# Kernel optimization log

Measured on AMD Instinct MI355X. Metric: run time of the kernel, lower is better.

Reference implementation:

```python
import jax, jax.numpy as jnp
import numpy as np

N = 6144          # active voxels / points
C = 96            # embed_channels
B = 2             # batch size
D = H = W = 32    # sparse spatial shape
K = 16            # PFAS kNN
DEPTH = 4
GRID_OPTS = np.array([[0.1, 0.1, 0.1], [0.4, 0.4, 0.4], [0.2, 0.2, 0.2]], dtype=np.float32)
BN_EPS = 1e-5


def _bn(x, g, b):
    # BatchNorm1d in training mode: batch stats over the point dim, biased var
    m = x.mean(0)
    v = jnp.var(x, axis=0)
    return (x - m) * jax.lax.rsqrt(v + BN_EPS) * g + b


def _seg_sum(x, seg):
    return jax.ops.segment_sum(x, seg, num_segments=N)


def _forward(indices, x, fp_w, fp_b, fp_g, fp_be, att_w1, att_b1, att_w2, att_b2,
             ff_w1, ff_b1, ff_g, ff_be, ff_w2, ff_b2, sa_w1, sa_b1, sa_w2, sa_b2,
             fj_w1, fj_b1, fj_g, fj_be, fj_w2, fj_b2,
             proj_w, proj_g, proj_be, lw_w, lw_g, lw_be, w_w, adp_w,
             fuse_w, fuse_g, fuse_be, conv1_w, bn1_g, bn1_be, conv2_w, bn2_g, bn2_be):
    # ---- CMPFE ----
    p = jax.nn.relu(_bn(x @ fp_w.T + fp_b, fp_g, fp_be))            # [N,9]
    cd, cl, nm = p[:, :3], p[:, 3:6], p[:, 6:9]

    def _att(f, i):
        h = jax.nn.relu(f @ att_w1[i].T + att_b1[i])
        return jax.nn.sigmoid(h @ att_w2[i].T + att_b2[i])

    enh = jnp.concatenate([cd, cl * _att(cl, 0), nm * _att(nm, 1)], axis=1)
    fu = jax.nn.relu(_bn(enh @ ff_w1.T + ff_b1, ff_g, ff_be)) @ ff_w2.T + ff_b2
    sem = jax.nn.sigmoid(jax.nn.relu(fu @ sa_w1.T + sa_b1) @ sa_w2.T + sa_b2)
    feat = fu * sem + x * (1.0 - sem)                               # new x.features

    # ---- PFAS: kNN geometry stats ----
    coord = indices[:, 1:].astype(jnp.float32)                      # [N,3]
    batch = indices[:, 0]
    sq = jnp.sum(coord * coord, axis=1)
    d2 = sq[:, None] + sq[None, :] - 2.0 * (coord @ coord.T)
    dist = jnp.sqrt(jnp.maximum(d2, 1e-12))
    same = batch[None, :] == batch[:, None]
    eye = jnp.eye(N, dtype=bool)
    dist = jnp.where(same & ~eye, dist, jnp.inf)
    neg_nd, idx = jax.lax.top_k(-dist, K)                           # K nearest
    nbr = coord[idx]                                                # [N,K,3]
    cent = nbr - nbr.mean(axis=1, keepdims=True)
    cov = jnp.einsum('nkd,nke->nde', cent, cent) / (K - 1)
    S = jnp.linalg.svd(cov, compute_uv=False)                       # [N,3] descending
    Sn = S / (S.sum(axis=1, keepdims=True) + 1e-6)
    linearity = Sn[:, 0:1] - (Sn[:, 1] + Sn[:, 2])[:, None]
    mean_dist = (-neg_nd).mean(axis=1, keepdims=True)
    density = 1.0 / (mean_dist + 1e-6)
    fl = jax.nn.relu(_bn(feat @ fj_w1.T + fj_b1, fj_g, fj_be)) @ fj_w2.T + fj_b2
    fp_ = jax.nn.softmax(fl, axis=1)
    tower = (density * 2.0 + fp_[:, 0:1]) / 3.0
    backg = (jnp.maximum(1.0 - linearity, 1.0 - density) + fp_[:, 1:2]) / 3.0
    line = (linearity * 2.0 + fp_[:, 2:3]) / 3.0
    go = jnp.asarray(GRID_OPTS)
    lg = go[2] * jnp.array([1.0, 1.0, 5.0], jnp.float32)            # last dim *5
    grid_sizes = tower * go[0] + backg * go[1] + line * lg + 1e-6   # [N,3]

    # ---- representative grids (N > 200 path) ----
    gm = grid_sizes.mean(axis=1)
    order = jnp.argsort(gm)
    reps = [grid_sizes[order[100:200]].mean(0),
            grid_sizes[order[::-1][:100]].mean(0),
            grid_sizes[order[:100]].mean(0)]

    # ---- voxel-grid clustering (torch_geometric voxel_grid + unique inverse) ----
    start = coord.min(axis=0)

    def _cluster(size):
        size = jnp.clip(size, 1e-6, None)
        c = jnp.clip(jnp.floor((coord - start) / size).astype(jnp.int64), 0, 4095)
        mx = c.max(axis=0) + 1
        ids = ((batch.astype(jnp.int64) * mx[0] + c[:, 0]) * mx[1] + c[:, 1]) * mx[2] + c[:, 2]
        _, inv = jnp.unique(ids, return_inverse=True, size=N, fill_value=0)
        return inv.reshape(-1)

    # ---- adaptive multi-branch scatter softmax aggregation ----
    branch_feats = []
    for i in range(DEPTH - 1):
        seg = _cluster(reps[i])
        cnt = jnp.maximum(_seg_sum(jnp.ones((N, 1), feat.dtype), seg), 1.0)
        pw = jax.nn.relu(_bn(feat @ lw_w[i].T, lw_g[i], lw_be[i]))
        pw = pw - (_seg_sum(pw, seg) / cnt)[seg]
        pw = pw @ w_w[i].T
        pw = jnp.exp(pw - pw.max())
        pw = pw / (_seg_sum(pw, seg)[seg] + 1e-6)
        pf = jax.nn.relu(_bn(feat @ proj_w[i].T, proj_g[i], proj_be[i])) * pw
        branch_feats.append(_seg_sum(pf, seg)[seg])
    adp = jax.nn.softmax(feat @ adp_w.T, axis=1)                    # [N,3]
    agg = jnp.einsum('nc,ncd->nd', adp, jnp.stack(branch_feats, 1))
    last = jax.nn.relu(_bn(feat @ proj_w[-1].T, proj_g[-1], proj_be[-1]))
    fused = jax.nn.relu(_bn(jnp.concatenate([last, agg], 1) @ fuse_w.T, fuse_g, fuse_be)) + feat
    res = fused

    # ---- submanifold sparse conv block (dense scatter form; inactive sites zero,
    #      outputs gathered only at active sites == SubMConv3d) ----
    bi, zi, yi, xi = indices[:, 0], indices[:, 1], indices[:, 2], indices[:, 3]

    def _subm(f, w):
        grid = jnp.zeros((B, D, H, W, C), f.dtype).at[bi, zi, yi, xi].set(f)
        o = jax.lax.conv_general_dilated(grid, w, (1, 1, 1), 'SAME',
                                         dimension_numbers=('NDHWC', 'DHWIO', 'NDHWC'))
        return o[bi, zi, yi, xi]

    f1 = jax.nn.relu(_bn(_subm(fused, conv1_w), bn1_g, bn1_be))
    f2 = _bn(_subm(f1, conv2_w), bn2_g, bn2_be)
    return jax.nn.relu(f2 + res)


def setup_inputs() -> dict:
    key = jax.random.key(0)
    ks = iter(jax.random.split(key, 64))

    def rn(*shape, s=0.05):
        return jax.random.normal(next(ks), shape, jnp.float32) * s

    # unique active voxel coordinates
    rng = np.random.default_rng(0)
    flat = rng.choice(B * D * H * W, size=N, replace=False)
    b = flat // (D * H * W)
    r = flat % (D * H * W)
    z = r // (H * W)
    y = (r % (H * W)) // W
    xw = r % W
    indices = jnp.asarray(np.stack([b, z, y, xw], 1).astype(np.int32))
    Ch = C // 2
    return {
        'x': jax.random.normal(next(ks), (N, C), jnp.float32),
        'indices': indices,
        'fp_w': rn(9, C), 'fp_b': rn(9), 'fp_g': jnp.ones(9), 'fp_be': jnp.zeros(9),
        'att_w1': rn(2, 16, 3), 'att_b1': rn(2, 16), 'att_w2': rn(2, 3, 16), 'att_b2': rn(2, 3),
        'ff_w1': rn(C, 9), 'ff_b1': rn(C), 'ff_g': jnp.ones(C), 'ff_be': jnp.zeros(C),
        'ff_w2': rn(C, C), 'ff_b2': rn(C),
        'sa_w1': rn(Ch, C), 'sa_b1': rn(Ch), 'sa_w2': rn(1, Ch), 'sa_b2': rn(1),
        'fj_w1': rn(64, C), 'fj_b1': rn(64), 'fj_g': jnp.ones(64), 'fj_be': jnp.zeros(64),
        'fj_w2': rn(3, 64), 'fj_b2': rn(3),
        'proj_w': rn(DEPTH, C, C), 'proj_g': jnp.ones((DEPTH, C)), 'proj_be': jnp.zeros((DEPTH, C)),
        'lw_w': rn(DEPTH - 1, C, C), 'lw_g': jnp.ones((DEPTH - 1, C)), 'lw_be': jnp.zeros((DEPTH - 1, C)),
        'w_w': rn(DEPTH - 1, C, C),
        'adp_w': rn(DEPTH - 1, C),
        'fuse_w': rn(C, 2 * C), 'fuse_g': jnp.ones(C), 'fuse_be': jnp.zeros(C),
        'conv1_w': rn(3, 3, 3, C, C), 'bn1_g': jnp.ones(C), 'bn1_be': jnp.zeros(C),
        'conv2_w': rn(3, 3, 3, C, C), 'bn2_g': jnp.ones(C), 'bn2_be': jnp.zeros(C),
    }


def reference(x, indices, fp_w, fp_b, fp_g, fp_be, att_w1, att_b1, att_w2, att_b2,
              ff_w1, ff_b1, ff_g, ff_be, ff_w2, ff_b2, sa_w1, sa_b1, sa_w2, sa_b2,
              fj_w1, fj_b1, fj_g, fj_be, fj_w2, fj_b2,
              proj_w, proj_g, proj_be, lw_w, lw_g, lw_be, w_w, adp_w,
              fuse_w, fuse_g, fuse_be, conv1_w, bn1_g, bn1_be, conv2_w, bn2_g, bn2_be):
    return _forward(indices, x, fp_w, fp_b, fp_g, fp_be, att_w1, att_b1, att_w2, att_b2,
                    ff_w1, ff_b1, ff_g, ff_be, ff_w2, ff_b2, sa_w1, sa_b1, sa_w2, sa_b2,
                    fj_w1, fj_b1, fj_g, fj_be, fj_w2, fj_b2,
                    proj_w, proj_g, proj_be, lw_w, lw_g, lw_be, w_w, adp_w,
                    fuse_w, fuse_g, fuse_be, conv1_w, bn1_g, bn1_be, conv2_w, bn2_g, bn2_be)
```

## Files before the change

### kernel.cpp

```cpp
#include <hip/hip_runtime.h>
#include <cstdint>

#define NPTS 6144
#define CH 96
#define NCELEM (NPTS*CH)
#define HTSZ 16384

__device__ __forceinline__ unsigned fenc(float f){
  unsigned u = __float_as_uint(f);
  return (u & 0x80000000u) ? ~u : (u | 0x80000000u);
}
__device__ __forceinline__ float fdec(unsigned u){
  unsigned b = (u & 0x80000000u) ? (u & 0x7FFFFFFFu) : ~u;
  return __uint_as_float(b);
}

__device__ void eig3(double a00,double a01,double a02,double a11,double a12,double a22,
                     double &e0,double &e1,double &e2){
  double p1 = a01*a01 + a02*a02 + a12*a12;
  double q = (a00+a11+a22)/3.0;
  double b00=a00-q, b11=a11-q, b22=a22-q;
  double p2 = b00*b00 + b11*b11 + b22*b22 + 2.0*p1;
  if (p2 <= 1e-300){ e0=e1=e2=q; return; }
  double pp = sqrt(p2/6.0);
// ... 300 lines not shown
            for (int t=15;t>0;--t){
              unsigned a = s[t-1], b = s[t];
              unsigned lo = a<b?a:b, hi = a<b?b:a;
              s[t-1]=lo; s[t]=hi;
            }
          }
        }
      }
    }
  }
  for (int m=32; m; m>>=1) cnt += __shfl_xor(cnt, m);
  if (cnt < 16){
    #pragma unroll
    for (int t=0;t<16;++t) s[t] = 0xFFFFFFFFu;
    for (int it=0; it<96; ++it){
      int j = lane + it*64;
      unsigned pc = pk[j];
      if (j != pid && (int)(pc>>15) == myb){
        int dz = (int)((pc>>10)&31) - mz;
        int dy = (int)((pc>>5)&31) - my_;
        int dx = (int)(pc&31) - mx_;
        unsigned d2 = (unsigned)(dz*dz + dy*dy + dx*dx);
        unsigned key = (d2<<13) | (unsigned)j;
        if (key < s[15]){
          s[15] = key;
          #pragma unroll
          for (int t=15;t>0;--t){
            unsigned a = s[t-1], b = s[t];
            unsigned lo = a<b?a:b, hi = a<b?b:a;
            s[t-1]=lo; s[t]=hi;
          }
        }
      }
    }
  }
  float sdist = 0.f;
  int sz=0,sy=0,sx=0,szz=0,syy=0,sxx=0,szy=0,szx=0,syx=0;
  for (int r=0;r<16;++r){
    unsigned m = s[0];
    #pragma unroll
    for (int w=32; w; w>>=1){
      unsigned o = (unsigned)__shfl_xor((int)m, w);
      m = m<o ? m : o;
    }
    bool own = (s[0] == m);
    #pragma unroll
    for (int t=0;t<15;++t) s[t] = own ? s[t+1] : s[t];
    if (own) s[15] = 0xFFFFFFFFu;
    unsigned idx = m & 8191u;
    unsigned d2 = m >> 13;
    sdist += sqrtf((float)d2);
    unsigned pc = pk[idx];
    int nz=(int)((pc>>10)&31), ny=(int)((pc>>5)&31), nx=(int)(pc&31);
    sz+=nz; sy+=ny; sx+=nx;
    szz+=nz*nz; syy+=ny*ny; sxx+=nx*nx; szy+=nz*ny; szx+=nz*nx; syx+=ny*nx;
  }
  if (lane == 0){
    double m0 = sz/16.0, m1 = sy/16.0, m2 = sx/16.0;
    float c00 = (float)(((double)szz - 16.0*m0*m0)/15.0);
    float c11 = (float)(((double)syy - 16.0*m1*m1)/15.0);
    float c22 = (float)(((double)sxx - 16.0*m2*m2)/15.0);
    float c01 = (float)(((double)szy - 16.0*m0*m1)/15.0);
    float c02 = (float)(((double)szx - 16.0*m0*m2)/15.0);
    float c12 = (float)(((double)syx - 16.0*m1*m2)/15.0);
    double e0,e1,e2;
    eig3((double)c00,(double)c01,(double)c02,(double)c11,(double)c12,(double)c22, e0,e1,e2);
    float s0 = (float)fabs(e0), s1 = (float)fabs(e1), s2 = (float)fabs(e2);
    float den = s0 + s1 + s2 + 1e-6f;
    float sn0 = s0/den, sn1 = s1/den, sn2 = s2/den;
    linearity[pid] = sn0 - (sn1 + sn2);
    float md = sdist * (1.f/16.f);
    density[pid] = 1.f/(md + 1e-6f);
  }
}

__global__ void k_geo(const float* __restrict__ t64, const float* __restrict__ st,
                      const float* __restrict__ fg, const float* __restrict__ fbe,
                      const float* __restrict__ w2, const float* __restrict__ b2,
                      const float* __restrict__ density, const float* __restrict__ linearity,
                      float* __restrict__ gsz, float* __restrict__ gm){
  int p = blockIdx.x*blockDim.x + threadIdx.x;
  if (p >= NPTS) return;
  float fl[3];
  #pragma unroll
  for (int o=0;o<3;++o) fl[o] = b2[o];
  for (int k=0;k<64;++k){
    float v = t64[(long)p*64+k];
    v = fmaxf((v - st[k*2])*st[k*2+1]*fg[k] + fbe[k], 0.f);
    #pragma unroll
    for (int o=0;o<3;++o) fl[o] = fmaf(v, w2[o*64+k], fl[o]);
  }
  float mx = fmaxf(fl[0], fmaxf(fl[1], fl[2]));
  float e0 = expf(fl[0]-mx), e1 = expf(fl[1]-mx), e2 = expf(fl[2]-mx);
  float es = e0+e1+e2;
  float p0 = e0/es, p1 = e1/es, p2 = e2/es;
  float den = density[p], lin = linearity[p];
  float tw = (den*2.f + p0)/3.f;
  float bg = (fmaxf(1.f-lin, 1.f-den) + p1)/3.f;
  float ln = (lin*2.f + p2)/3.f;
  float g0 = tw*0.1f + bg*0.4f + ln*0.2f + 1e-6f;
  float g1 = tw*0.1f + bg*0.4f + ln*0.2f + 1e-6f;
  float g2 = tw*0.1f + bg*0.4f + ln*1.0f + 1e-6f;
  gsz[p*3+0]=g0; gsz[p*3+1]=g1; gsz[p*3+2]=g2;
  gm[p] = (g0+g1+g2)/3.f;
}

#define RNKCHUNK 768
__global__ void __launch_bounds__(256) k_rank(const float* __restrict__ gm, int* __restrict__ rank){
  __shared__ unsigned long long lk[RNKCHUNK];
  int j0 = blockIdx.y*RNKCHUNK;
  for (int i=threadIdx.x; i<RNKCHUNK; i+=256){
    int j = j0 + i;
    lk[i] = (((unsigned long long)fenc(gm[j]))<<13) | (unsigned long long)j;
  }
  __syncthreads();
  int p = blockIdx.x*256 + threadIdx.x;
  unsigned long long myk = (((unsigned long long)fenc(gm[p]))<<13) | (unsigned long long)p;
  int cnt = 0;
  #pragma unroll 4
  for (int i=0; i<RNKCHUNK; ++i) cnt += (lk[i] < myk) ? 1 : 0;
  atomicAdd(&rank[p], cnt);
}
__global__ void k_scatter(const int* __restrict__ rank, const float* __restrict__ gsz,
                          float* __restrict__ bkt){
  int p = blockIdx.x*blockDim.x + threadIdx.x;
  if (p >= NPTS) return;
  int r = rank[p];
  int z = -1, t = 0;
  if (r < 100){ z = 2; t = r; }
  else if (r < 200){ z = 0; t = r - 100; }
  else if (r >= NPTS-100){ z = 1; t = r - (NPTS-100); }
  if (z >= 0){
    #pragma unroll
    for (int d=0; d<3; ++d) bkt[(z*100 + t)*3 + d] = gsz[p*3+d];
  }
}
__global__ void k_reps(const float* __restrict__ bkt, float* __restrict__ reps){
  int i = threadIdx.x;
  if (i >= 9) return;
  int z = i/3, d = i - z*3;
  double s = 0.0;
  for (int t=0; t<100; ++t) s += (double)bkt[(z*100 + t)*3 + d];
  reps[i] = (float)(s/100.0);
}

__global__ void k_cluster_c(const int* __restrict__ ind, const float* __restrict__ reps,
                            const int* __restrict__ startmin, int* __restrict__ cbuf, int* mxbuf){
  int z = blockIdx.y;
  int p = blockIdx.x*blockDim.x + threadIdx.x;
  __shared__ int lmx[3];
  if (threadIdx.x < 3) lmx[threadIdx.x] = 0;
  __syncthreads();
  if (p < NPTS){
    #pragma unroll
    for (int d=0; d<3; ++d){
      float sizev = fmaxf(reps[z*3+d], 1e-6f);
      float cf = floorf(((float)ind[p*4+1+d] - (float)startmin[d]) / sizev);
      int ci = (int)cf;
      ci = ci < 0 ? 0 : (ci > 4095 ? 4095 : ci);
      cbuf[((long)z*NPTS + p)*3 + d] = ci;
      atomicMax(&lmx[d], ci);
    }
  }
  __syncthreads();
  if (threadIdx.x < 3) atomicMax(&mxbuf[z*3+threadIdx.x], lmx[threadIdx.x]);
}
__global__ void k_cluster_ids(const int* __restrict__ ind, const int* __restrict__ cbuf,
                              const int* __restrict__ mxbuf, long long* __restrict__ ids){
  int z = blockIdx.y;
  int p = blockIdx.x*blockDim.x + threadIdx.x;
  if (p >= NPTS) return;
  long long mx0 = mxbuf[z*3+0]+1, mx1 = mxbuf[z*3+1]+1, mx2 = mxbuf[z*3+2]+1;
  long long b = ind[p*4];
  const int* cc = cbuf + ((long)z*NPTS + p)*3;
  ids[(long)z*NPTS + p] = ((b*mx0 + cc[0])*mx1 + cc[1])*mx2 + cc[2];
}

__device__ __forceinline__ int ht_hash(unsigned long long id){
  unsigned long long h = id * 0x9E3779B97F4A7C15ull;
  return (int)(h >> 49) & (HTSZ-1);
}
__global__ void k_seg_build(const long long* __restrict__ ids,
                            unsigned long long* __restrict__ keys, int* __restrict__ vals){
  int z = blockIdx.y;
  int p = blockIdx.x*blockDim.x + threadIdx.x;
  if (p >= NPTS) return;
  unsigned long long id = (unsigned long long)ids[(long)z*NPTS + p];
  unsigned long long* K = keys + (long)z*HTSZ;
  int* V = vals + (long)z*HTSZ;
  int slot = ht_hash(id);
  while (true){
    unsigned long long prev = atomicCAS(&K[slot], ~0ull, id);
    if (prev == ~0ull || prev == id){ atomicMin(&V[slot], p); break; }
    slot = (slot + 1) & (HTSZ-1);
  }
}
__global__ void k_seg_lookup(const long long* __restrict__ ids,
                             const unsigned long long* __restrict__ keys, const int* __restrict__ vals,
                             int* __restrict__ seg, int* __restrict__ cnt){
  int z = blockIdx.y;
  int p = blockIdx.x*blockDim.x + threadIdx.x;
  if (p >= NPTS) return;
  unsigned long long id = (unsigned long long)ids[(long)z*NPTS + p];
  const unsigned long long* K = keys + (long)z*HTSZ;
  int slot = ht_hash(id);
  while (K[slot] != id) slot = (slot + 1) & (HTSZ-1);
  int rep = vals[(long)z*HTSZ + slot];
  seg[(long)z*NPTS + p] = rep;
  atomicAdd(&cnt[(long)z*NPTS + rep], 1);
}

__global__ void k_pw_accum(const float* __restrict__ tlw, const float* __restrict__ stats,
                           const float* __restrict__ g, const float* __restrict__ be,
                           const int* __restrict__ seg, float* __restrict__ S){
  int z = blockIdx.y;
  int idx = blockIdx.x*blockDim.x + threadIdx.x;
  int p = idx/CH, c = idx - p*CH;
  const float* st = stats + z*192;
  float v = tlw[(long)z*NCELEM + idx];
  v = fmaxf((v - st[c*2])*st[c*2+1]*g[z*CH+c] + be[z*CH+c], 0.f);
  atomicAdd(&S[(long)z*NCELEM + (long)seg[(long)z*NPTS+p]*CH + c], v);
}
__global__ void k_exp_accum(const float* __restrict__ pw2, const unsigned* __restrict__ maxenc,
                            const int* __restrict__ seg, float* __restrict__ E){
  int z = blockIdx.y;
  int idx = blockIdx.x*blockDim.x + threadIdx.x;
  int p = idx/CH, c = idx - p*CH;
  float mv = fdec(maxenc[z]);
  float v = expf(pw2[(long)z*NCELEM + idx] - mv);
  atomicAdd(&E[(long)z*NCELEM + (long)seg[(long)z*NPTS+p]*CH + c], v);
}
__global__ void k_pf_accum(const float* __restrict__ tp, const float* __restrict__ stats,
                           const float* __restrict__ pg, const float* __restrict__ pbe,
                           const float* __restrict__ pw2, const unsigned* __restrict__ maxenc,
                           const int* __restrict__ seg, const float* __restrict__ E,
                           float* __restrict__ F){
  int z = blockIdx.y;
  int idx = blockIdx.x*blockDim.x + threadIdx.x;
  int p = idx/CH, c = idx - p*CH;
  const float* st = stats + z*192;
  float v = tp[(long)z*NCELEM + idx];
  v = fmaxf((v - st[c*2])*st[c*2+1]*pg[z*CH+c] + pbe[z*CH+c], 0.f);
  float mv = fdec(maxenc[z]);
  int sg = seg[(long)z*NPTS+p];
  float w = expf(pw2[(long)z*NCELEM + idx] - mv) / (E[(long)z*NCELEM + (long)sg*CH + c] + 1e-6f);
  atomicAdd(&F[(long)z*NCELEM + (long)sg*CH + c], v*w);
}
__global__ void k_adp(const float* __restrict__ feat, const float* __restrict__ aw,
                      float* __restrict__ adp){
  int p = blockIdx.x*blockDim.x + threadIdx.x;
  if (p >= NPTS) return;
  float a0=0.f, a1=0.f, a2=0.f;
  for (int k=0;k<CH;++k){
    float f = feat[(long)p*CH+k];
    a0 = fmaf(f, aw[k], a0);
    a1 = fmaf(f, aw[CH+k], a1);
    a2 = fmaf(f, aw[2*CH+k], a2);
  }
  float m = fmaxf(a0, fmaxf(a1,a2));
  float e0 = expf(a0-m), e1 = expf(a1-m), e2 = expf(a2-m);
  float s = e0+e1+e2;
  adp[p*3]=e0/s; adp[p*3+1]=e1/s; adp[p*3+2]=e2/s;
}
__global__ void k_agg(const float* __restrict__ adp, const float* __restrict__ F,
                      const int* __restrict__ seg, float* __restrict__ agg){
  int idx = blockIdx.x*blockDim.x + threadIdx.x;
  int p = idx/CH, c = idx - p*CH;
  float s = 0.f;
  #pragma unroll
  for (int z=0;z<3;++z)
    s = fmaf(adp[p*3+z], F[(long)z*NCELEM + (long)seg[(long)z*NPTS+p]*CH + c], s);
  agg[idx] = s;
}

__global__ void k_fused(const float* __restrict__ tf, const float* __restrict__ st,
                        const float* __restrict__ fg, const float* __restrict__ fbe,
                        const float* __restrict__ feat, float* __restrict__ fused){
  int idx = blockIdx.x*blockDim.x + threadIdx.x;
  int c = idx % CH;
  float v = tf[idx];
  v = fmaxf((v - st[c*2])*st[c*2+1]*fg[c] + fbe[c], 0.f);
  fused[idx] = v + feat[idx];
}
__global__ void k_table(const int* __restrict__ ind, int* __restrict__ table){
  int p = blockIdx.x*blockDim.x + threadIdx.x;
  if (p >= NPTS) return;
  int b = ind[p*4], z = ind[p*4+1], y = ind[p*4+2], x = ind[p*4+3];
  table[((b*32+z)*32+y)*32+x] = p;
}
__global__ void k_nbr(const int* __restrict__ ind, const int* __restrict__ table,
                      int* __restrict__ nbrtab){
  int idx = blockIdx.x*blockDim.x + threadIdx.x;
  if (idx >= NPTS*27) return;
  int p = idx/27, tap = idx - p*27;
  int dz = tap/9 - 1;
  int rm = tap % 9;
  int dy = rm/3 - 1, dx = rm%3 - 1;
  int b = ind[p*4], z = ind[p*4+1]+dz, y = ind[p*4+2]+dy, x = ind[p*4+3]+dx;
  int q = -1;
  if ((unsigned)z < 32u && (unsigned)y < 32u && (unsigned)x < 32u)
    q = table[((b*32+z)*32+y)*32+x];
  nbrtab[idx] = q;
}
__global__ void __launch_bounds__(256) k_convlist(const int* __restrict__ nbrtab,
                                                  int* __restrict__ tapcnt,
                                                  int* __restrict__ ptlist){
  __shared__ int lcnt[27], lbase[27], lpos[27];
  int tid = threadIdx.x;
  if (tid < 27){ lcnt[tid] = 0; lpos[tid] = 0; }
  __syncthreads();
  int base = blockIdx.x * 6912;
  for (int i = tid; i < 6912; i += 256){
    int idx = base + i;
    if (nbrtab[idx] >= 0) atomicAdd(&lcnt[idx % 27], 1);
  }
  __syncthreads();
  if (tid < 27) lbase[tid] = atomicAdd(&tapcnt[tid], lcnt[tid]);
  __syncthreads();
  for (int i = tid; i < 6912; i += 256){
    int idx = base + i;
    int q = nbrtab[idx];
    if (q >= 0){
      int tap = idx % 27;
      int p = idx / 27;
      int pos = lbase[tap] + atomicAdd(&lpos[tap], 1);
      ptlist[tap*NPTS + pos] = (p<<16) | q;
    }
  }
}
__global__ void __launch_bounds__(256) k_conv_gemm(
    const float* __restrict__ src, const float* __restrict__ Wc,
    const int* __restrict__ tapcnt, const int* __restrict__ ptlist,
    float* __restrict__ out){
  int tap = blockIdx.y;
  int n = tapcnt[tap];
  int r0 = blockIdx.x*32;
  if (r0 >= n) return;
  __shared__ float Al[32*97];
  __shared__ float Wl[96*97];
  __shared__ int pqs[32];
  int tid = threadIdx.x;
  if (tid < 32){
    int r = r0 + tid;
    pqs[tid] = (r < n) ? ptlist[tap*NPTS + r] : -1;
  }
  __syncthreads();
  for (int idx4 = tid; idx4 < 2304; idx4 += 256){
    int ci = idx4/24, c4 = idx4 - ci*24;
    float4 w = ((const float4*)(Wc + ((long)tap*96 + ci)*96))[c4];
    float* d = &Wl[ci*97 + c4*4];
    d[0]=w.x; d[1]=w.y; d[2]=w.z; d[3]=w.w;
  }
  for (int idx4 = tid; idx4 < 32*24; idx4 += 256){
    int ir = idx4/24, c4 = idx4 - ir*24;
    int pq = pqs[ir];
    float4 s = make_float4(0.f,0.f,0.f,0.f);
    if (pq >= 0){
      int q = pq & 0xFFFF;
      s = ((const float4*)(src + (long)q*CH))[c4];
    }
    float* d = &Al[ir*97 + c4*4];
    d[0]=s.x; d[1]=s.y; d[2]=s.z; d[3]=s.w;
  }
  __syncthreads();
  int rp = tid >> 4, cg = tid & 15;
  int co0 = cg*6;
  int ra = 2*rp, rb = ra+1;
  float acc0[6]={0,0,0,0,0,0}, acc1[6]={0,0,0,0,0,0};
  for (int k=0;k<96;++k){
    float a0 = Al[ra*97+k], a1 = Al[rb*97+k];
    #pragma unroll
    for (int j=0;j<6;++j){
      float w = Wl[k*97+co0+j];
      acc0[j] = fmaf(a0, w, acc0[j]);
      acc1[j] = fmaf(a1, w, acc1[j]);
    }
  }
  int pa = pqs[ra], pb = pqs[rb];
  if (pa >= 0){
    float* o = out + (long)(pa>>16)*CH + co0;
    #pragma unroll
    for (int j=0;j<6;++j) atomicAdd(&o[j], acc0[j]);
  }
  if (pb >= 0){
    float* o = out + (long)(pb>>16)*CH + co0;
    #pragma unroll
    for (int j=0;j<6;++j) atomicAdd(&o[j], acc1[j]);
  }
}
__global__ void k_bnrelu(const float* __restrict__ a, const float* __restrict__ st,
                         const float* __restrict__ g, const float* __restrict__ be,
                         float* __restrict__ o){
  int idx = blockIdx.x*blockDim.x + threadIdx.x;
  int c = idx % CH;
  float v = a[idx];
  o[idx] = fmaxf((v - st[c*2])*st[c*2+1]*g[c] + be[c], 0.f);
}
__global__ void k_final(const float* __restrict__ c2, const float* __restrict__ st,
                        const float* __restrict__ g, const float* __restrict__ be,
                        const float* __restrict__ fused, float* __restrict__ out){
  int idx = blockIdx.x*blockDim.x + threadIdx.x;
  int c = idx % CH;
  float v = c2[idx];
  v = (v - st[c*2])*st[c*2+1]*g[c] + be[c];
  out[idx] = fmaxf(v + fused[idx], 0.f);
}

extern "C" void kernel_launch(void* const* d_in, const int* in_sizes, int n_in,
                              void* d_out, int out_size, void* d_ws, size_t ws_size,
                              hipStream_t stream)
{
  const float* x      = (const float*)d_in[0];
  const int*   ind    = (const int*)  d_in[1];
  const float* fp_w   = (const float*)d_in[2];
  const float* fp_b   = (const float*)d_in[3];
  const float* fp_g   = (const float*)d_in[4];
  const float* fp_be  = (const float*)d_in[5];
  const float* att_w1 = (const float*)d_in[6];
  const float* att_b1 = (const float*)d_in[7];
  const float* att_w2 = (const float*)d_in[8];
  const float* att_b2 = (const float*)d_in[9];
  const float* ff_w1  = (const float*)d_in[10];
  const float* ff_b1  = (const float*)d_in[11];
  const float* ff_g   = (const float*)d_in[12];
  const float* ff_be  = (const float*)d_in[13];
  const float* ff_w2  = (const float*)d_in[14];
  const float* ff_b2  = (const float*)d_in[15];
  const float* sa_w1  = (const float*)d_in[16];
  const float* sa_b1  = (const float*)d_in[17];
  const float* sa_w2  = (const float*)d_in[18];
  const float* sa_b2  = (const float*)d_in[19];
  const float* fj_w1  = (const float*)d_in[20];
  const float* fj_b1  = (const float*)d_in[21];
  const float* fj_g   = (const float*)d_in[22];
  const float* fj_be  = (const float*)d_in[23];
  const float* fj_w2  = (const float*)d_in[24];
  const float* fj_b2  = (const float*)d_in[25];
  const float* proj_w = (const float*)d_in[26];
  const float* proj_g = (const float*)d_in[27];
  const float* proj_be= (const float*)d_in[28];
  const float* lw_w   = (const float*)d_in[29];
  const float* lw_g   = (const float*)d_in[30];
  const float* lw_be  = (const float*)d_in[31];
  const float* w_w    = (const float*)d_in[32];
  const float* adp_w  = (const float*)d_in[33];
  const float* fuse_w = (const float*)d_in[34];
  const float* fuse_g = (const float*)d_in[35];
  const float* fuse_be= (const float*)d_in[36];
  const float* conv1_w= (const float*)d_in[37];
  const float* bn1_g  = (const float*)d_in[38];
  const float* bn1_be = (const float*)d_in[39];
  const float* conv2_w= (const float*)d_in[40];
  const float* bn2_g  = (const float*)d_in[41];
  const float* bn2_be = (const float*)d_in[42];
  float* outp = (float*)d_out;
  (void)in_sizes; (void)n_in; (void)out_size; (void)ws_size;

  char* ws = (char*)d_ws;
  size_t off = 0;
  auto alloc = [&](size_t bytes)->size_t{
    off = (off + 255) & ~(size_t)255;
    size_t o = off; off += bytes; return o;
  };
  const size_t FNC = (size_t)NCELEM*4;
  size_t o_packed = alloc((size_t)NPTS*4);
  size_t o_start  = alloc(16);
  size_t o_dens   = alloc((size_t)NPTS*4);
  size_t o_lin    = alloc((size_t)NPTS*4);
  size_t o_t9     = alloc((size_t)NPTS*9*4);
  size_t o_enh    = alloc((size_t)NPTS*9*4);
  size_t o_gm     = alloc((size_t)NPTS*4);
  size_t o_gsz    = alloc((size_t)NPTS*3*4);
  size_t o_reps   = alloc(16*4);
  size_t o_bkt    = alloc((size_t)3*100*3*4);
  size_t o_cbuf   = alloc((size_t)3*NPTS*3*4);
  size_t o_ids    = alloc((size_t)3*NPTS*8);
  size_t o_seg    = alloc((size_t)3*NPTS*4);
  size_t o_adp    = alloc((size_t)NPTS*3*4);
  size_t o_table  = alloc((size_t)65536*4);
  size_t o_nbr    = alloc((size_t)NPTS*27*4);
  size_t o_ptlist = alloc((size_t)27*NPTS*4);
  size_t o_t64    = alloc((size_t)NPTS*64*4);
  size_t o_stats  = alloc((size_t)13*192*4);
  size_t o_htk    = alloc((size_t)3*HTSZ*8);
  size_t o_htv    = alloc((size_t)3*HTSZ*4);
  size_t o_S      = alloc(3*FNC);
  size_t o_E      = alloc(3*FNC);
  size_t o_F      = alloc(3*FNC);
  size_t o_c1     = alloc(FNC);
  size_t o_c2     = alloc(FNC);
  size_t o_cnt    = alloc((size_t)3*NPTS*4);
  size_t o_rank   = alloc((size_t)NPTS*4);
  size_t o_tapcnt = alloc(32*4);
  size_t o_mx     = alloc(16*4);
  size_t o_maxenc = alloc(16*4);
  size_t zend = off;
  size_t o_T96 = alloc(FNC);
  size_t o_fu  = alloc(FNC);
  size_t o_feat= alloc(FNC);
  size_t o_tlw = alloc(3*FNC);
  size_t o_pw2 = alloc(3*FNC);
  size_t o_tp  = alloc(4*FNC);
  size_t o_agg = alloc(FNC);
  size_t o_tf  = alloc(FNC);
  size_t o_fsd = alloc(FNC);
  size_t o_f1  = alloc(FNC);

  float* stats = (float*)(ws + o_stats);
  long zcount = (long)((zend - o_S)/4);

  k_zero<<<dim3(2048), dim3(256), 0, stream>>>((int*)(ws+o_S), zcount);
  k_init<<<dim3(256), dim3(256), 0, stream>>>((int*)(ws+o_table), (int*)(ws+o_start));
  k_htinit<<<dim3((3*HTSZ+255)/256), dim3(256), 0, stream>>>((unsigned long long*)(ws+o_htk), (int*)(ws+o_htv));
  k_pack_min<<<dim3(24), dim3(256), 0, stream>>>(ind, (unsigned*)(ws+o_packed), (int*)(ws+o_start));
  k_table<<<dim3(24), 256, 0, stream>>>(ind, (int*)(ws+o_table));

  k_mm<<<dim3(192,1), 256, 0, stream>>>(x, fp_w, fp_b, (float*)(ws+o_t9), 96, 9,
      0,0,0,0, nullptr,0, nullptr,nullptr,0, nullptr,nullptr,nullptr, nullptr, 0);
  k_stats<<<dim3(9,1), 256, 0, stream>>>((float*)(ws+o_t9), 0, 9, stats+0*192, 0);
  k_p_att_enh<<<dim3(24), 256, 0, stream>>>((float*)(ws+o_t9), stats+0*192, fp_g, fp_be,
      att_w1, att_b1, att_w2, att_b2, (float*)(ws+o_enh));

  k_mm<<<dim3(192,1), 256, 0, stream>>>((float*)(ws+o_enh), ff_w1, ff_b1, (float*)(ws+o_T96), 9, 96,
      0,0,0,0, nullptr,0, nullptr,nullptr,0, nullptr,nullptr,nullptr, nullptr, 0);
  k_stats<<<dim3(96,1), 256, 0, stream>>>((float*)(ws+o_T96), 0, 96, stats+1*192, 0);
  k_mm<<<dim3(192,1), 256, 0, stream>>>((float*)(ws+o_T96), ff_w2, ff_b2, (float*)(ws+o_fu), 96, 96,
      0,0,0,0, stats+1*192,0, ff_g, ff_be,0, nullptr,nullptr,nullptr, nullptr, 1);

  k_sem_feat<<<dim3(1536), 256, 0, stream>>>((float*)(ws+o_fu), x, sa_w1, sa_b1, sa_w2, sa_b2,
      (float*)(ws+o_feat));

  k_knn<<<dim3(1536), 256, 0, stream>>>((unsigned*)(ws+o_packed), (int*)(ws+o_table),
      (float*)(ws+o_dens), (float*)(ws+o_lin));

  k_mm<<<dim3(192,1), 256, 0, stream>>>((float*)(ws+o_feat), fj_w1, fj_b1, (float*)(ws+o_t64), 96, 64,
      0,0,0,0, nullptr,0, nullptr,nullptr,0, nullptr,nullptr,nullptr, nullptr, 0);
  k_stats<<<dim3(64,1), 256, 0, stream>>>((float*)(ws+o_t64), 0, 64, stats+2*192, 0);
  k_geo<<<dim3(24), 256, 0, stream>>>((float*)(ws+o_t64), stats+2*192, fj_g, fj_be, fj_w2, fj_b2,
      (float*)(ws+o_dens), (float*)(ws+o_lin), (float*)(ws+o_gsz), (float*)(ws+o_gm));

  k_rank<<<dim3(24,8), 256, 0, stream>>>((float*)(ws+o_gm), (int*)(ws+o_rank));
  k_scatter<<<dim3(24), 256, 0, stream>>>((int*)(ws+o_rank), (float*)(ws+o_gsz), (float*)(ws+o_bkt));
  k_reps<<<dim3(1), 64, 0, stream>>>((float*)(ws+o_bkt), (float*)(ws+o_reps));

  k_cluster_c<<<dim3(24,3), 256, 0, stream>>>(ind, (float*)(ws+o_reps), (int*)(ws+o_start),
      (int*)(ws+o_cbuf), (int*)(ws+o_mx));
  k_cluster_ids<<<dim3(24,3), 256, 0, stream>>>(ind, (int*)(ws+o_cbuf), (int*)(ws+o_mx),
      (long long*)(ws+o_ids));
  k_seg_build<<<dim3(24,3), 256, 0, stream>>>((long long*)(ws+o_ids),
      (unsigned long long*)(ws+o_htk), (int*)(ws+o_htv));
  k_seg_lookup<<<dim3(24,3), 256, 0, stream>>>((long long*)(ws+o_ids),
      (unsigned long long*)(ws+o_htk), (int*)(ws+o_htv), (int*)(ws+o_seg), (int*)(ws+o_cnt));

  k_mm<<<dim3(192,3), 256, 0, stream>>>((float*)(ws+o_feat), lw_w, nullptr, (float*)(ws+o_tlw), 96, 96,
      0, 96*96, NCELEM, 0, nullptr,0, nullptr,nullptr,0, nullptr,nullptr,nullptr, nullptr, 0);
  k_stats<<<dim3(96,3), 256, 0, stream>>>((float*)(ws+o_tlw), NCELEM, 96, stats+3*192, 192);
  k_pw_accum<<<dim3(2304,3), 256, 0, stream>>>((float*)(ws+o_tlw), stats+3*192, lw_g, lw_be,
      (int*)(ws+o_seg), (float*)(ws+o_S));
  k_mm<<<dim3(192,3), 256, 0, stream>>>((float*)(ws+o_tlw), w_w, nullptr, (float*)(ws+o_pw2), 96, 96,
      NCELEM, 96*96, NCELEM, 0, stats+3*192,192, lw_g, lw_be,96,
      (float*)(ws+o_S), (int*)(ws+o_seg), (int*)(ws+o_cnt), (unsigned*)(ws+o_maxenc), 2);
  k_exp_accum<<<dim3(2304,3), 256, 0, stream>>>((float*)(ws+o_pw2), (unsigned*)(ws+o_maxenc),
      (int*)(ws+o_seg), (float*)(ws+o_E));
  k_mm<<<dim3(192,4), 256, 0, stream>>>((float*)(ws+o_feat), proj_w, nullptr, (float*)(ws+o_tp), 96, 96,
      0, 96*96, NCELEM, 0, nullptr,0, nullptr,nullptr,0, nullptr,nullptr,nullptr, nullptr, 0);
  k_stats<<<dim3(96,4), 256, 0, stream>>>((float*)(ws+o_tp), NCELEM, 96, stats+6*192, 192);
  k_pf_accum<<<dim3(2304,3), 256, 0, stream>>>((float*)(ws+o_tp), stats+6*192, proj_g, proj_be,
      (float*)(ws+o_pw2), (unsigned*)(ws+o_maxenc), (int*)(ws+o_seg), (float*)(ws+o_E), (float*)(ws+o_F));
  k_adp<<<dim3(24), 256, 0, stream>>>((float*)(ws+o_feat), adp_w, (float*)(ws+o_adp));
  k_agg<<<dim3(2304), 256, 0, stream>>>((float*)(ws+o_adp), (float*)(ws+o_F), (int*)(ws+o_seg),
      (float*)(ws+o_agg));

  k_mm_fuse<<<dim3(192), 256, 0, stream>>>((float*)(ws+o_tp) + (size_t)3*NCELEM, stats+9*192,
      proj_g + 3*96, proj_be + 3*96, (float*)(ws+o_agg), fuse_w, (float*)(ws+o_tf));
  k_stats<<<dim3(96,1), 256, 0, stream>>>((float*)(ws+o_tf), 0, 96, stats+10*192, 0);
  k_fused<<<dim3(2304), 256, 0, stream>>>((float*)(ws+o_tf), stats+10*192, fuse_g, fuse_be,
      (float*)(ws+o_feat), (float*)(ws+o_fsd));

  k_nbr<<<dim3((NPTS*27+255)/256), 256, 0, stream>>>(ind, (int*)(ws+o_table), (int*)(ws+o_nbr));
  k_convlist<<<dim3(24), 256, 0, stream>>>((int*)(ws+o_nbr), (int*)(ws+o_tapcnt),
      (int*)(ws+o_ptlist));
  k_conv_gemm<<<dim3(192,27), 256, 0, stream>>>((float*)(ws+o_fsd), conv1_w,
      (int*)(ws+o_tapcnt), (int*)(ws+o_ptlist), (float*)(ws+o_c1));
  k_stats<<<dim3(96,1), 256, 0, stream>>>((float*)(ws+o_c1), 0, 96, stats+11*192, 0);
  k_bnrelu<<<dim3(2304), 256, 0, stream>>>((float*)(ws+o_c1), stats+11*192, bn1_g, bn1_be, (float*)(ws+o_f1));
  k_conv_gemm<<<dim3(192,27), 256, 0, stream>>>((float*)(ws+o_f1), conv2_w,
      (int*)(ws+o_tapcnt), (int*)(ws+o_ptlist), (float*)(ws+o_c2));
  k_stats<<<dim3(96,1), 256, 0, stream>>>((float*)(ws+o_c2), 0, 96, stats+12*192, 0);
  k_final<<<dim3(2304), 256, 0, stream>>>((float*)(ws+o_c2), stats+12*192, bn2_g, bn2_be,
      (float*)(ws+o_fsd), outp);
}
```

Measured before the change: 543.9 us.

## Replace scatter-atomic tap-list sparse conv with output-stationary gather conv

The sparse 3x3x3 convolution no longer builds per-tap point lists and scatters results with float atomics. Each block now owns 16 output points, loops over all 27 taps, gathers neighbour rows and the tap weight slice into shared memory, and accumulates in registers before a plain store. This removes the list-building kernel, the atomics and the zeroing of the conv outputs, which now sit outside the zeroed region. The cost is that every block reloads the full 96x96 weight slice for each active tap, giving far more weight traffic, and the grid shrinks to 384 blocks with one row per thread.

```diff
diff --git a/kernel.cpp b/kernel.cpp
--- a/kernel.cpp
+++ b/kernel.cpp
@@ -626,91 +626,54 @@
     q = table[((b*32+z)*32+y)*32+x];
   nbrtab[idx] = q;
 }
-__global__ void __launch_bounds__(256) k_convlist(const int* __restrict__ nbrtab,
-                                                  int* __restrict__ tapcnt,
-                                                  int* __restrict__ ptlist){
-  __shared__ int lcnt[27], lbase[27], lpos[27];
+__global__ void __launch_bounds__(256) k_conv_os(
+    const float* __restrict__ src, const float* __restrict__ Wc,
+    const int* __restrict__ nbrtab, float* __restrict__ out){
+  __shared__ float Al[16*97];
+  __shared__ float Wl[96*97];
+  __shared__ int qrow[16];
+  __shared__ int anyv;
   int tid = threadIdx.x;
-  if (tid < 27){ lcnt[tid] = 0; lpos[tid] = 0; }
-  __syncthreads();
-  int base = blockIdx.x * 6912;
-  for (int i = tid; i < 6912; i += 256){
-    int idx = base + i;
-    if (nbrtab[idx] >= 0) atomicAdd(&lcnt[idx % 27], 1);
-  }
-  __syncthreads();
-  if (tid < 27) lbase[tid] = atomicAdd(&tapcnt[tid], lcnt[tid]);
-  __syncthreads();
-  for (int i = tid; i < 6912; i += 256){
-    int idx = base + i;
-    int q = nbrtab[idx];
-    if (q >= 0){
-      int tap = idx % 27;
-      int p = idx / 27;
-      int pos = lbase[tap] + atomicAdd(&lpos[tap], 1);
-      ptlist[tap*NPTS + pos] = (p<<16) | q;
-    }
-  }
-}
-__global__ void __launch_bounds__(256) k_conv_gemm(
-    const float* __restrict__ src, const float* __restrict__ Wc,
-    const int* __restrict__ tapcnt, const int* __restrict__ ptlist,
-    float* __restrict__ out){
-  int tap = blockIdx.y;
-  int n = tapcnt[tap];
-  int r0 = blockIdx.x*32;
-  if (r0 >= n) return;
-  __shared__ float Al[32*97];
-  __shared__ float Wl[96*97];
-  __shared__ int pqs[32];
-  int tid = threadIdx.x;
-  if (tid < 32){
-    int r = r0 + tid;
-    pqs[tid] = (r < n) ? ptlist[tap*NPTS + r] : -1;
-  }
-  __syncthreads();
-  for (int idx4 = tid; idx4 < 2304; idx4 += 256){
-    int ci = idx4/24, c4 = idx4 - ci*24;
-    float4 w = ((const float4*)(Wc + ((long)tap*96 + ci)*96))[c4];
-    float* d = &Wl[ci*97 + c4*4];
-    d[0]=w.x; d[1]=w.y; d[2]=w.z; d[3]=w.w;
-  }
-  for (int idx4 = tid; idx4 < 32*24; idx4 += 256){
-    int ir = idx4/24, c4 = idx4 - ir*24;
-    int pq = pqs[ir];
-    float4 s = make_float4(0.f,0.f,0.f,0.f);
-    if (pq >= 0){
-      int q = pq & 0xFFFF;
-      s = ((const float4*)(src + (long)q*CH))[c4];
-    }
-    float* d = &Al[ir*97 + c4*4];
-    d[0]=s.x; d[1]=s.y; d[2]=s.z; d[3]=s.w;
-  }
-  __syncthreads();
+  int p0 = blockIdx.x*16;
   int rp = tid >> 4, cg = tid & 15;
   int co0 = cg*6;
-  int ra = 2*rp, rb = ra+1;
-  float acc0[6]={0,0,0,0,0,0}, acc1[6]={0,0,0,0,0,0};
-  for (int k=0;k<96;++k){
-    float a0 = Al[ra*97+k], a1 = Al[rb*97+k];
-    #pragma unroll
-    for (int j=0;j<6;++j){
-      float w = Wl[k*97+co0+j];
-      acc0[j] = fmaf(a0, w, acc0[j]);
-      acc1[j] = fmaf(a1, w, acc1[j]);
-    }
-  }
-  int pa = pqs[ra], pb = pqs[rb];
-  if (pa >= 0){
-    float* o = out + (long)(pa>>16)*CH + co0;
-    #pragma unroll
-    for (int j=0;j<6;++j) atomicAdd(&o[j], acc0[j]);
-  }
-  if (pb >= 0){
-    float* o = out + (long)(pb>>16)*CH + co0;
-    #pragma unroll
-    for (int j=0;j<6;++j) atomicAdd(&o[j], acc1[j]);
-  }
+  float acc[6] = {0,0,0,0,0,0};
+  for (int tap=0; tap<27; ++tap){
+    if (tid == 0) anyv = 0;
+    __syncthreads();
+    if (tid < 16){
+      int q = nbrtab[(p0+tid)*27 + tap];
+      qrow[tid] = q;
+      if (q >= 0) atomicOr(&anyv, 1);
+    }
+    __syncthreads();
+    if (anyv){
+      for (int i4 = tid; i4 < 2304; i4 += 256){
+        int ci = i4/24, c4 = i4 - ci*24;
+        float4 w = ((const float4*)(Wc + ((long)tap*96 + ci)*96))[c4];
+        float* d = &Wl[ci*97 + c4*4];
+        d[0]=w.x; d[1]=w.y; d[2]=w.z; d[3]=w.w;
+      }
+      for (int i4 = tid; i4 < 16*24; i4 += 256){
+        int ir = i4/24, c4 = i4 - ir*24;
+        int q = qrow[ir];
+        float4 s = make_float4(0.f,0.f,0.f,0.f);
+        if (q >= 0) s = ((const float4*)(src + (long)q*CH))[c4];
+        float* d = &Al[ir*97 + c4*4];
+        d[0]=s.x; d[1]=s.y; d[2]=s.z; d[3]=s.w;
+      }
+      __syncthreads();
+      for (int k=0;k<96;++k){
+        float a = Al[rp*97+k];
+        #pragma unroll
+        for (int j=0;j<6;++j) acc[j] = fmaf(a, Wl[k*97+co0+j], acc[j]);
+      }
+      __syncthreads();
+    }
+  }
+  float* o = out + (long)(p0+rp)*CH + co0;
+  #pragma unroll
+  for (int j=0;j<6;++j) o[j] = acc[j];
 }
 __global__ void k_bnrelu(const float* __restrict__ a, const float* __restrict__ st,
                          const float* __restrict__ g, const float* __restrict__ be,
@@ -803,7 +766,6 @@
   size_t o_adp    = alloc((size_t)NPTS*3*4);
   size_t o_table  = alloc((size_t)65536*4);
   size_t o_nbr    = alloc((size_t)NPTS*27*4);
-  size_t o_ptlist = alloc((size_t)27*NPTS*4);
   size_t o_t64    = alloc((size_t)NPTS*64*4);
   size_t o_stats  = alloc((size_t)13*192*4);
   size_t o_htk    = alloc((size_t)3*HTSZ*8);
@@ -811,11 +773,8 @@
   size_t o_S      = alloc(3*FNC);
   size_t o_E      = alloc(3*FNC);
   size_t o_F      = alloc(3*FNC);
-  size_t o_c1     = alloc(FNC);
-  size_t o_c2     = alloc(FNC);
   size_t o_cnt    = alloc((size_t)3*NPTS*4);
   size_t o_rank   = alloc((size_t)NPTS*4);
-  size_t o_tapcnt = alloc(32*4);
   size_t o_mx     = alloc(16*4);
   size_t o_maxenc = alloc(16*4);
   size_t zend = off;
@@ -828,7 +787,9 @@
   size_t o_agg = alloc(FNC);
   size_t o_tf  = alloc(FNC);
   size_t o_fsd = alloc(FNC);
+  size_t o_c1  = alloc(FNC);
   size_t o_f1  = alloc(FNC);
+  size_t o_c2  = alloc(FNC);
 
   float* stats = (float*)(ws + o_stats);
   long zcount = (long)((zend - o_S)/4);
@@ -902,14 +863,12 @@
       (float*)(ws+o_feat), (float*)(ws+o_fsd));
 
   k_nbr<<<dim3((NPTS*27+255)/256), 256, 0, stream>>>(ind, (int*)(ws+o_table), (int*)(ws+o_nbr));
-  k_convlist<<<dim3(24), 256, 0, stream>>>((int*)(ws+o_nbr), (int*)(ws+o_tapcnt),
-      (int*)(ws+o_ptlist));
-  k_conv_gemm<<<dim3(192,27), 256, 0, stream>>>((float*)(ws+o_fsd), conv1_w,
-      (int*)(ws+o_tapcnt), (int*)(ws+o_ptlist), (float*)(ws+o_c1));
+  k_conv_os<<<dim3(NPTS/16), 256, 0, stream>>>((float*)(ws+o_fsd), conv1_w,
+      (int*)(ws+o_nbr), (float*)(ws+o_c1));
   k_stats<<<dim3(96,1), 256, 0, stream>>>((float*)(ws+o_c1), 0, 96, stats+11*192, 0);
   k_bnrelu<<<dim3(2304), 256, 0, stream>>>((float*)(ws+o_c1), stats+11*192, bn1_g, bn1_be, (float*)(ws+o_f1));
-  k_conv_gemm<<<dim3(192,27), 256, 0, stream>>>((float*)(ws+o_f1), conv2_w,
-      (int*)(ws+o_tapcnt), (int*)(ws+o_ptlist), (float*)(ws+o_c2));
+  k_conv_os<<<dim3(NPTS/16), 256, 0, stream>>>((float*)(ws+o_f1), conv2_w,
+      (int*)(ws+o_nbr), (float*)(ws+o_c2));
   k_stats<<<dim3(96,1), 256, 0, stream>>>((float*)(ws+o_c2), 0, 96, stats+12*192, 0);
   k_final<<<dim3(2304), 256, 0, stream>>>((float*)(ws+o_c2), stats+12*192, bn2_g, bn2_be,
       (float*)(ws+o_fsd), outp);
```

New measurement: 767.8 us. 41.2% more time.

## Replace atomic scatter in sparse conv with per-tap partial buffer and gather-sum

Applied to the files above, without the earlier changes.

The sparse 3x3x3 convolution GEMM now writes each tap's output row into a dedicated [point, tap, channel] partial buffer instead of atomically adding into the output. A new gather kernel then sums the valid taps per point using the neighbour table. This removes float atomics and the zeroing pass, and makes the sum order deterministic. In exchange it writes and rereads a 27x-sized intermediate (about 64 MB), with an atomic fallback when the workspace is too small.

```diff
diff --git a/kernel.cpp b/kernel.cpp
--- a/kernel.cpp
+++ b/kernel.cpp
@@ -653,6 +653,81 @@
   }
 }
 __global__ void __launch_bounds__(256) k_conv_gemm(
+    const float* __restrict__ src, const float* __restrict__ Wc,
+    const int* __restrict__ tapcnt, const int* __restrict__ ptlist,
+    float* __restrict__ part){
+  int tap = blockIdx.y;
+  int n = tapcnt[tap];
+  int r0 = blockIdx.x*32;
+  if (r0 >= n) return;
+  __shared__ float Al[32*97];
+  __shared__ float Wl[96*97];
+  __shared__ int pqs[32];
+  int tid = threadIdx.x;
+  if (tid < 32){
+    int r = r0 + tid;
+    pqs[tid] = (r < n) ? ptlist[tap*NPTS + r] : -1;
+  }
+  __syncthreads();
+  for (int idx4 = tid; idx4 < 2304; idx4 += 256){
+    int ci = idx4/24, c4 = idx4 - ci*24;
+    float4 w = ((const float4*)(Wc + ((long)tap*96 + ci)*96))[c4];
+    float* d = &Wl[ci*97 + c4*4];
+    d[0]=w.x; d[1]=w.y; d[2]=w.z; d[3]=w.w;
+  }
+  for (int idx4 = tid; idx4 < 32*24; idx4 += 256){
+    int ir = idx4/24, c4 = idx4 - ir*24;
+    int pq = pqs[ir];
+    float4 s = make_float4(0.f,0.f,0.f,0.f);
+    if (pq >= 0){
+      int q = pq & 0xFFFF;
+      s = ((const float4*)(src + (long)q*CH))[c4];
+    }
+    float* d = &Al[ir*97 + c4*4];
+    d[0]=s.x; d[1]=s.y; d[2]=s.z; d[3]=s.w;
+  }
+  __syncthreads();
+  int rp = tid >> 4, cg = tid & 15;
+  int co0 = cg*6;
+  int ra = 2*rp, rb = ra+1;
+  float acc0[6]={0,0,0,0,0,0}, acc1[6]={0,0,0,0,0,0};
+  for (int k=0;k<96;++k){
+    float a0 = Al[ra*97+k], a1 = Al[rb*97+k];
+    #pragma unroll
+    for (int j=0;j<6;++j){
+      float w = Wl[k*97+co0+j];
+      acc0[j] = fmaf(a0, w, acc0[j]);
+      acc1[j] = fmaf(a1, w, acc1[j]);
+    }
+  }
+  int pa = pqs[ra], pb = pqs[rb];
+  if (pa >= 0){
+    float* o = part + ((long)(pa>>16)*27 + tap)*CH + co0;
+    #pragma unroll
+    for (int j=0;j<6;++j) o[j] = acc0[j];
+  }
+  if (pb >= 0){
+    float* o = part + ((long)(pb>>16)*27 + tap)*CH + co0;
+    #pragma unroll
+    for (int j=0;j<6;++j) o[j] = acc1[j];
+  }
+}
+__global__ void __launch_bounds__(256) k_conv_sum(const int* __restrict__ nbrtab,
+                                                  const float* __restrict__ part,
+                                                  float* __restrict__ out){
+  int idx = blockIdx.x*256 + threadIdx.x;
+  int p = idx/24, c4 = idx - p*24;
+  const int* nt = nbrtab + p*27;
+  float4 acc = make_float4(0.f,0.f,0.f,0.f);
+  for (int tap=0; tap<27; ++tap){
+    if (nt[tap] >= 0){
+      float4 v = ((const float4*)part)[((long)p*27 + tap)*24 + c4];
+      acc.x += v.x; acc.y += v.y; acc.z += v.z; acc.w += v.w;
+    }
+  }
+  ((float4*)out)[idx] = acc;
+}
+__global__ void __launch_bounds__(256) k_conv_gemm_atomic(
     const float* __restrict__ src, const float* __restrict__ Wc,
     const int* __restrict__ tapcnt, const int* __restrict__ ptlist,
     float* __restrict__ out){
@@ -778,7 +853,7 @@
   const float* bn2_g  = (const float*)d_in[41];
   const float* bn2_be = (const float*)d_in[42];
   float* outp = (float*)d_out;
-  (void)in_sizes; (void)n_in; (void)out_size; (void)ws_size;
+  (void)in_sizes; (void)n_in; (void)out_size;
 
   char* ws = (char*)d_ws;
   size_t off = 0;
@@ -811,8 +886,6 @@
   size_t o_S      = alloc(3*FNC);
   size_t o_E      = alloc(3*FNC);
   size_t o_F      = alloc(3*FNC);
-  size_t o_c1     = alloc(FNC);
-  size_t o_c2     = alloc(FNC);
   size_t o_cnt    = alloc((size_t)3*NPTS*4);
   size_t o_rank   = alloc((size_t)NPTS*4);
   size_t o_tapcnt = alloc(32*4);
@@ -828,7 +901,13 @@
   size_t o_agg = alloc(FNC);
   size_t o_tf  = alloc(FNC);
   size_t o_fsd = alloc(FNC);
+  size_t o_c1  = alloc(FNC);
   size_t o_f1  = alloc(FNC);
+  size_t o_c2  = alloc(FNC);
+  size_t need_base = off;
+  size_t o_part = alloc((size_t)NPTS*27*CH*4);
+  bool use_part = (off <= ws_size);
+  (void)need_base;
 
   float* stats = (float*)(ws + o_stats);
   long zcount = (long)((zend - o_S)/4);
@@ -904,12 +983,28 @@
   k_nbr<<<dim3((NPTS*27+255)/256), 256, 0, stream>>>(ind, (int*)(ws+o_table), (int*)(ws+o_nbr));
   k_convlist<<<dim3(24), 256, 0, stream>>>((int*)(ws+o_nbr), (int*)(ws+o_tapcnt),
       (int*)(ws+o_ptlist));
-  k_conv_gemm<<<dim3(192,27), 256, 0, stream>>>((float*)(ws+o_fsd), conv1_w,
-      (int*)(ws+o_tapcnt), (int*)(ws+o_ptlist), (float*)(ws+o_c1));
+  if (use_part){
+    k_conv_gemm<<<dim3(192,27), 256, 0, stream>>>((float*)(ws+o_fsd), conv1_w,
+        (int*)(ws+o_tapcnt), (int*)(ws+o_ptlist), (float*)(ws+o_part));
+    k_conv_sum<<<dim3(NPTS*24/256), 256, 0, stream>>>((int*)(ws+o_nbr), (float*)(ws+o_part),
+        (float*)(ws+o_c1));
+  } else {
+    k_zero<<<dim3(2304), dim3(256), 0, stream>>>((int*)(ws+o_c1), NCELEM);
+    k_conv_gemm_atomic<<<dim3(192,27), 256, 0, stream>>>((float*)(ws+o_fsd), conv1_w,
+        (int*)(ws+o_tapcnt), (int*)(ws+o_ptlist), (float*)(ws+o_c1));
+  }
   k_stats<<<dim3(96,1), 256, 0, stream>>>((float*)(ws+o_c1), 0, 96, stats+11*192, 0);
   k_bnrelu<<<dim3(2304), 256, 0, stream>>>((float*)(ws+o_c1), stats+11*192, bn1_g, bn1_be, (float*)(ws+o_f1));
-  k_conv_gemm<<<dim3(192,27), 256, 0, stream>>>((float*)(ws+o_f1), conv2_w,
-      (int*)(ws+o_tapcnt), (int*)(ws+o_ptlist), (float*)(ws+o_c2));
+  if (use_part){
+    k_conv_gemm<<<dim3(192,27), 256, 0, stream>>>((float*)(ws+o_f1), conv2_w,
+        (int*)(ws+o_tapcnt), (int*)(ws+o_ptlist), (float*)(ws+o_part));
+    k_conv_sum<<<dim3(NPTS*24/256), 256, 0, stream>>>((int*)(ws+o_nbr), (float*)(ws+o_part),
+        (float*)(ws+o_c2));
+  } else {
+    k_zero<<<dim3(2304), dim3(256), 0, stream>>>((int*)(ws+o_c2), NCELEM);
+    k_conv_gemm_atomic<<<dim3(192,27), 256, 0, stream>>>((float*)(ws+o_f1), conv2_w,
+        (int*)(ws+o_tapcnt), (int*)(ws+o_ptlist), (float*)(ws+o_c2));
+  }
   k_stats<<<dim3(96,1), 256, 0, stream>>>((float*)(ws+o_c2), 0, 96, stats+12*192, 0);
   k_final<<<dim3(2304), 256, 0, stream>>>((float*)(ws+o_c2), stats+12*192, bn2_g, bn2_be,
       (float*)(ws+o_fsd), outp);
```

Measured after the change: 506.4 us. 6.9% less time.
